# Kernel optimization log

Hardware: AMD Instinct MI355X
Metric: run time of the kernel (lower is better)

The kernel has to match this reference:

```python
import jax, jax.numpy as jnp
import numpy as np

B, H, W, C = 32, 56, 56, 192
WS, SH = 7, 3            # window size, shift size
NH = 6                   # num heads
HD = C // NH             # head dim = 32
N = WS * WS              # tokens per window = 49
NW = (H // WS) * (W // WS)  # windows per image = 64
HID = int(C * 4.0)       # MLP hidden = 768
EPS = 1e-6               # flax LayerNorm default


def _rel_index():
    # (N, N) int index into the (2*WS-1)^2 relative position bias table
    coords = np.stack(np.meshgrid(np.arange(WS), np.arange(WS), indexing='ij')).reshape(2, -1)
    rel = coords[:, :, None] - coords[:, None, :]          # (2, N, N)
    rel = rel.transpose(1, 2, 0) + (WS - 1)                # shift to >= 0
    idx = rel[..., 0] * (2 * WS - 1) + rel[..., 1]
    return jnp.asarray(idx, jnp.int32)


def _attn_mask():
    # standard Swin shifted-window mask: -100 between different regions
    img = np.zeros((H, W))
    cnt = 0
    for hs in (slice(0, -WS), slice(-WS, -SH), slice(-SH, None)):
        for ws in (slice(0, -WS), slice(-WS, -SH), slice(-SH, None)):
            img[hs, ws] = cnt
            cnt += 1
    win = img.reshape(H // WS, WS, W // WS, WS).transpose(0, 2, 1, 3).reshape(NW, N)
    diff = win[:, None, :] - win[:, :, None]
    return jnp.asarray(np.where(diff != 0, -100.0, 0.0), jnp.float32)


def setup_inputs() -> dict:
    key = jax.random.key(0)
    ks = jax.random.split(key, 8)
    s = 0.02
    return {
        'x': jax.random.normal(ks[0], (B, H, W, C), jnp.float32),
        'mask': _attn_mask(),
        'rel_index': _rel_index(),
        'ln1_scale': jnp.ones((C,), jnp.float32),
        'ln1_bias': jnp.zeros((C,), jnp.float32),
        'qkv_w': jax.random.normal(ks[1], (C, 3 * C), jnp.float32) * s,
        'qkv_b': jnp.zeros((3 * C,), jnp.float32),
        'rpb_table': jax.random.normal(ks[2], ((2 * WS - 1) ** 2, NH), jnp.float32) * s,
        'proj_w': jax.random.normal(ks[3], (C, C), jnp.float32) * s,
        'proj_b': jnp.zeros((C,), jnp.float32),
        'ln2_scale': jnp.ones((C,), jnp.float32),
        'ln2_bias': jnp.zeros((C,), jnp.float32),
        'mlp_w1': jax.random.normal(ks[4], (C, HID), jnp.float32) * s,
        'mlp_b1': jnp.zeros((HID,), jnp.float32),
        'mlp_w2': jax.random.normal(ks[5], (HID, C), jnp.float32) * s,
        'mlp_b2': jnp.zeros((C,), jnp.float32),
    }


def _ln(x, scale, bias):
    mu = jnp.mean(x, axis=-1, keepdims=True)
    var = jnp.mean(jnp.square(x - mu), axis=-1, keepdims=True)
    return (x - mu) * jax.lax.rsqrt(var + EPS) * scale + bias


def reference(x, mask, rel_index, ln1_scale, ln1_bias, qkv_w, qkv_b, rpb_table,
              proj_w, proj_b, ln2_scale, ln2_bias, mlp_w1, mlp_b1, mlp_w2, mlp_b2):
    # ---- W-MSA branch ----
    y = _ln(x, ln1_scale, ln1_bias)
    # cyclic shift (grid divisible by window -> pad_to_blocks is a no-op)
    y = jnp.roll(y, shift=(-SH, -SH), axis=(1, 2))
    # window partition: (B,H,W,C) -> (B*NW, N, C)
    y = y.reshape(B, H // WS, WS, W // WS, WS, C).transpose(0, 1, 3, 2, 4, 5)
    y = y.reshape(B * NW, N, C)
    # qkv: (B*NW, N, 3, NH, HD) -> q,k,v each (B*NW, NH, N, HD)
    qkv = (y @ qkv_w + qkv_b).reshape(B * NW, N, 3, NH, HD).transpose(2, 0, 3, 1, 4)
    q, k, v = qkv[0], qkv[1], qkv[2]
    attn = jnp.einsum('bhnd,bhmd->bhnm', q, k) * (HD ** -0.5)
    # relative position bias: (N,N,NH) -> (1,NH,N,N)
    attn = attn + rpb_table[rel_index].transpose(2, 0, 1)[None]
    # shifted-window mask: broadcast over batch and heads
    attn = attn.reshape(B, NW, NH, N, N) + mask[None, :, None]
    attn = jax.nn.softmax(attn.reshape(B * NW, NH, N, N), axis=-1)
    y = jnp.einsum('bhnm,bhmd->bhnd', attn, v).transpose(0, 2, 1, 3).reshape(B * NW, N, C)
    y = y @ proj_w + proj_b
    # window reverse and un-shift
    y = y.reshape(B, H // WS, W // WS, WS, WS, C).transpose(0, 1, 3, 2, 4, 5).reshape(B, H, W, C)
    y = jnp.roll(y, shift=(SH, SH), axis=(1, 2))
    x = x + y
    # ---- MLP branch ----
    z = _ln(x, ln2_scale, ln2_bias)
    z = jax.nn.gelu(z @ mlp_w1 + mlp_b1)  # flax nn.gelu default (tanh approx)
    z = z @ mlp_w2 + mlp_b2
    return x + z
```

## Files before the change

kernel.cpp:

```cpp
#include <hip/hip_runtime.h>


typedef __bf16 bf16_t;
typedef __bf16 bf16x8 __attribute__((ext_vector_type(8)));
typedef float  f32x4  __attribute__((ext_vector_type(4)));

__device__ inline float wred_sum(float v) {
#pragma unroll
  for (int o = 32; o; o >>= 1) v += __shfl_xor(v, o);
  return v;
}

__device__ inline float gelu_tanh(float x) {
  float u = 0.7978845608028654f * (x + 0.044715f * x * x * x);
  float e = __expf(2.f * u);
  float t = 1.f - 2.f / (e + 1.f);
  return 0.5f * x * (1.f + t);
}

__global__ __launch_bounds__(256) void k_ln1_win(
    const float* __restrict__ x, const float* __restrict__ sc,
    const float* __restrict__ bi, bf16_t* __restrict__ yw, int b0, int nTok) {
  int wv = (int)((blockIdx.x * 256 + threadIdx.x) >> 6);
  int lane = threadIdx.x & 63;
  if (wv >= nTok) return;
  int winL = wv / 49;
  int t = wv - winL * 49;
  int wi = winL & 63;
  int b = b0 + (winL >> 6);
  int t7 = t / 7;
  int hr = (wi >> 3) * 7 + t7;
  int wr = (wi & 7) * 7 + (t - t7 * 7);
  int h = hr + 3; if (h >= 56) h -= 56;
  int w = wr + 3; if (w >= 56) w -= 56;
  const float* xp = x + (((size_t)(b * 56 + h)) * 56 + w) * 192;
  float v0 = xp[lane], v1 = xp[lane + 64], v2 = xp[lane + 128];
  float s = wred_sum(v0 + v1 + v2);
  float q = wred_sum(v0 * v0 + v1 * v1 + v2 * v2);
  float mu = s * (1.f / 192.f);
  float var = q * (1.f / 192.f) - mu * mu;
  float rs = rsqrtf(var + 1e-6f);
  bf16_t* op = yw + (size_t)wv * 192;
  op[lane]       = (bf16_t)((v0 - mu) * rs * sc[lane]       + bi[lane]);
  op[lane + 64]  = (bf16_t)((v1 - mu) * rs * sc[lane + 64]  + bi[lane + 64]);
  op[lane + 128] = (bf16_t)((v2 - mu) * rs * sc[lane + 128] + bi[lane + 128]);
}

__global__ __launch_bounds__(256) void k_transpose_cvt(
    const float* __restrict__ in, bf16_t* __restrict__ out, int K, int N) {
  int idx = blockIdx.x * 256 + threadIdx.x;
  if (idx >= K * N) return;
  int n = idx / K, k = idx - n * K;
  out[idx] = (bf16_t)in[(size_t)k * N + n];
}

template <int K>
__global__ __launch_bounds__(256, 2) void k_gemm_bs(
    const bf16_t* __restrict__ A, const bf16_t* __restrict__ Bt,
    const float* __restrict__ bias, bf16_t* __restrict__ C, int Nn, int nMt) {
  constexpr int NKS = K / 32;
  int tid = threadIdx.x;
  int w = tid >> 6, lane = tid & 63;
  int c = lane & 15, g = lane >> 4;
  int bn = blockIdx.x;
  bf16x8 bf[4][NKS];
  const bf16_t* bp = Bt + (size_t)(bn * 64 + c) * K + 8 * g;
#pragma unroll
  for (int jc = 0; jc < 4; ++jc)
#pragma unroll
    for (int ks = 0; ks < NKS; ++ks)
      bf[jc][ks] = *(const bf16x8*)(bp + (size_t)jc * 16 * K + 32 * ks);
  float4 bias4[4];
#pragma unroll
  for (int jc = 0; jc < 4; ++jc)
    bias4[jc] = *(const float4*)(bias + bn * 64 + jc * 16 + 4 * g);
  for (int mt = blockIdx.y; mt < nMt; mt += gridDim.y) {
    int m0 = mt * 256 + w * 64;
    f32x4 acc[4][4] = {};
    const bf16_t* ap = A + (size_t)(m0 + c) * K + 8 * g;
#pragma unroll
    for (int ks = 0; ks < NKS; ++ks) {
      bf16x8 af[4];
#pragma unroll
      for (int ir = 0; ir < 4; ++ir)
        af[ir] = *(const bf16x8*)(ap + (size_t)ir * 16 * K + 32 * ks);
#pragma unroll
      for (int jc = 0; jc < 4; ++jc)
#pragma unroll
        for (int ir = 0; ir < 4; ++ir)
          acc[jc][ir] = __builtin_amdgcn_mfma_f32_16x16x32_bf16(
              bf[jc][ks], af[ir], acc[jc][ir], 0, 0, 0);
    }
#pragma unroll
    for (int ir = 0; ir < 4; ++ir) {
      bf16_t* cp = C + (size_t)(m0 + ir * 16 + c) * Nn + bn * 64 + 4 * g;
#pragma unroll
      for (int jc = 0; jc < 4; ++jc) {
        union { uint2 u; bf16_t e[4]; } pk;
#pragma unroll
        for (int r = 0; r < 4; ++r)
          pk.e[r] = (bf16_t)(acc[jc][ir][r] + ((const float*)&bias4[jc])[r]);
        *(uint2*)(cp + jc * 16) = pk.u;
      }
    }
  }
}

__global__ __launch_bounds__(64) void k_attn(
    const bf16_t* __restrict__ qkv, const int* __restrict__ relidx,
    const float* __restrict__ rpb, const float* __restrict__ mask,
    bf16_t* __restrict__ attn_out) {
  __shared__ char sm[8192];
  int blk = blockIdx.x;
  int wL = blk / 6, h = blk - wL * 6;
  int lane = threadIdx.x;
  int c = lane & 15, g = lane >> 4;
  {
    const float* mw = mask + (size_t)(wL & 63) * 2401;
    __bf16* bl = (__bf16*)sm;
    for (int idx = lane; idx < 2401; idx += 64)
      bl[idx] = (__bf16)(rpb[relidx[idx] * 6 + h] + mw[idx]);
  }
  const bf16_t* baseq = qkv + (size_t)wL * (49 * 576);
  f32x4 s[4][4] = {};
  bf16x8 qf[4], kf[4];
#pragma unroll
  for (int i = 0; i < 4; ++i) {
    int n = c + 16 * i; if (n > 48) n = 48;
    qf[i] = *(const bf16x8*)(baseq + (size_t)n * 576 + h * 32 + g * 8);
  }
#pragma unroll
  for (int j = 0; j < 4; ++j) {
    int m = c + 16 * j; if (m > 48) m = 48;
    kf[j] = *(const bf16x8*)(baseq + (size_t)m * 576 + 192 + h * 32 + g * 8);
  }
#pragma unroll
  for (int i = 0; i < 4; ++i)
#pragma unroll
    for (int j = 0; j < 4; ++j)
      s[i][j] = __builtin_amdgcn_mfma_f32_16x16x32_bf16(qf[i], kf[j], s[i][j],
                                                        0, 0, 0);
  const __bf16* bl = (const __bf16*)sm;
  float mxv[4][4], sum[4][4];
#pragma unroll
  for (int i = 0; i < 4; ++i)
#pragma unroll
    for (int r = 0; r < 4; ++r) {
      int n = 16 * i + 4 * g + r;
      int nc = n > 48 ? 48 : n;
      float best = -1e30f;
#pragma unroll
      for (int j = 0; j < 4; ++j) {
        int m = 16 * j + c;
        float v = -1e30f;
        if (m < 49)
          v = s[i][j][r] * 0.17677669529663687f + (float)bl[nc * 49 + m];
        s[i][j][r] = v;
        best = fmaxf(best, v);
      }
      mxv[i][r] = best;
    }
#pragma unroll
  for (int o = 8; o; o >>= 1)
#pragma unroll
    for (int i = 0; i < 4; ++i)
#pragma unroll
      for (int r = 0; r < 4; ++r)
        mxv[i][r] = fmaxf(mxv[i][r], __shfl_xor(mxv[i][r], o));
#pragma unroll
  for (int i = 0; i < 4; ++i)
#pragma unroll
    for (int r = 0; r < 4; ++r) {
      float ss = 0.f;
#pragma unroll
      for (int j = 0; j < 4; ++j) {
        float p = __expf(s[i][j][r] - mxv[i][r]);
        s[i][j][r] = p;
        ss += p;
      }
      sum[i][r] = ss;
    }
#pragma unroll
  for (int o = 8; o; o >>= 1)
#pragma unroll
    for (int i = 0; i < 4; ++i)
#pragma unroll
      for (int r = 0; r < 4; ++r)
        sum[i][r] += __shfl_xor(sum[i][r], o);
#pragma unroll
  for (int i = 0; i < 4; ++i)
#pragma unroll
    for (int j = 0; j < 4; ++j)
#pragma unroll
      for (int r = 0; r < 4; ++r) {
        int n = 16 * i + 4 * g + r;
        int m = 16 * j + c;
        int offb = n * 128 + ((2 * m) ^ ((n & 7) << 4));
        *(__bf16*)(sm + offb) = (__bf16)s[i][j][r];
      }
  f32x4 o2[4][2] = {};
#pragma unroll
  for (int kt = 0; kt < 2; ++kt) {
    bf16x8 pf[4], vf[2];
#pragma unroll
    for (int i = 0; i < 4; ++i) {
      int n = c + 16 * i;
      int cb = (16 * g + 64 * kt) ^ ((n & 7) << 4);
      pf[i] = *(const bf16x8*)(sm + n * 128 + cb);
    }
#pragma unroll
    for (int dt = 0; dt < 2; ++dt) {
      int d = c + 16 * dt;
      union { bf16x8 v; __bf16 e[8]; } u;
#pragma unroll
      for (int e0 = 0; e0 < 8; ++e0) {
        int m = 8 * g + e0 + 32 * kt; if (m > 48) m = 48;
        u.e[e0] = baseq[(size_t)m * 576 + 384 + h * 32 + d];
      }
      vf[dt] = u.v;
    }
#pragma unroll
    for (int i = 0; i < 4; ++i)
#pragma unroll
      for (int dt = 0; dt < 2; ++dt)
        o2[i][dt] = __builtin_amdgcn_mfma_f32_16x16x32_bf16(pf[i], vf[dt],
                                                            o2[i][dt], 0, 0, 0);
  }
#pragma unroll
  for (int i = 0; i < 4; ++i)
#pragma unroll
    for (int dt = 0; dt < 2; ++dt)
#pragma unroll
      for (int r = 0; r < 4; ++r) {
        int n = 16 * i + 4 * g + r;
        if (n < 49) {
          int d = 16 * dt + c;
          attn_out[((size_t)wL * 49 + n) * 192 + h * 32 + d] =
              (bf16_t)(o2[i][dt][r] / sum[i][r]);
        }
      }
}

__global__ __launch_bounds__(256) void k_unwin_ln2(
    const float* __restrict__ x, const bf16_t* __restrict__ projw,
    const float* __restrict__ sc, const float* __restrict__ bi,
    float* __restrict__ out, bf16_t* __restrict__ z, int b0, int nTok) {
  int wv = (int)((blockIdx.x * 256 + threadIdx.x) >> 6);
  int lane = threadIdx.x & 63;
  if (wv >= nTok) return;
  int bL = wv / 3136;
  int rem = wv - bL * 3136;
  int hh = rem / 56, ww2 = rem - hh * 56;
  int b = b0 + bL;
  int hr = hh + 53; if (hr >= 56) hr -= 56;
  int wr = ww2 + 53; if (wr >= 56) wr -= 56;
  int winL = bL * 64 + (hr / 7) * 8 + (wr / 7);
  int t = (hr % 7) * 7 + (wr % 7);
  const bf16_t* pp = projw + ((size_t)winL * 49 + t) * 192;
  size_t gtok = ((size_t)(b * 56 + hh)) * 56 + ww2;
  const float* xp = x + gtok * 192;
  float v0 = xp[lane]       + (float)pp[lane];
  float v1 = xp[lane + 64]  + (float)pp[lane + 64];
  float v2 = xp[lane + 128] + (float)pp[lane + 128];
  float* op = out + gtok * 192;
  op[lane] = v0; op[lane + 64] = v1; op[lane + 128] = v2;
  float s = wred_sum(v0 + v1 + v2);
  float q = wred_sum(v0 * v0 + v1 * v1 + v2 * v2);
  float mu = s * (1.f / 192.f);
  float var = q * (1.f / 192.f) - mu * mu;
  float rs = rsqrtf(var + 1e-6f);
  bf16_t* zp = z + gtok * 192;
  zp[lane]       = (bf16_t)((v0 - mu) * rs * sc[lane]       + bi[lane]);
  zp[lane + 64]  = (bf16_t)((v1 - mu) * rs * sc[lane + 64]  + bi[lane + 64]);
  zp[lane + 128] = (bf16_t)((v2 - mu) * rs * sc[lane + 128] + bi[lane + 128]);
}

__global__ __launch_bounds__(256, 2) void k_mlp_fused(
    const bf16_t* __restrict__ z, const bf16_t* __restrict__ w1T,
    const float* __restrict__ b1, const bf16_t* __restrict__ w2T,
    const float* __restrict__ b2, float* __restrict__ out) {
  __shared__ char hsm[128 * 256];
  int tid = threadIdx.x;
  int w = tid >> 6, lane = tid & 63;
  int c = lane & 15, g = lane >> 4;
  int wr = w >> 1, wc = w & 1;
  int m0 = blockIdx.x * 128;
  f32x4 acc2[6][4] = {};
  for (int hc = 0; hc < 6; ++hc) {
    f32x4 acc1[4][4] = {};
    const bf16_t* zp = z + (size_t)(m0 + wr * 64 + c) * 192 + 8 * g;
    const bf16_t* w1p = w1T + (size_t)(hc * 128 + wc * 64 + c) * 192 + 8 * g;
#pragma unroll
    for (int ks = 0; ks < 6; ++ks) {
      bf16x8 zf[4], wf[4];
#pragma unroll
      for (int i = 0; i < 4; ++i) {
        zf[i] = *(const bf16x8*)(zp + (size_t)i * 16 * 192 + 32 * ks);
        wf[i] = *(const bf16x8*)(w1p + (size_t)i * 16 * 192 + 32 * ks);
      }
#pragma unroll
      for (int jh = 0; jh < 4; ++jh)
#pragma unroll
        for (int ir = 0; ir < 4; ++ir)
          acc1[jh][ir] = __builtin_amdgcn_mfma_f32_16x16x32_bf16(
              wf[jh], zf[ir], acc1[jh][ir], 0, 0, 0);
    }
    if (hc) __syncthreads();
#pragma unroll
    for (int jh = 0; jh < 4; ++jh) {
      float4 b1v = *(const float4*)(b1 + hc * 128 + wc * 64 + jh * 16 + 4 * g);
#pragma unroll
      for (int ir = 0; ir < 4; ++ir) {
        union { uint2 u; __bf16 e[4]; } pk;
#pragma unroll
        for (int r = 0; r < 4; ++r)
          pk.e[r] = (__bf16)gelu_tanh(acc1[jh][ir][r] + ((const float*)&b1v)[r]);
        int row = wr * 64 + ir * 16 + c;
        int byo = (wc * 64 + jh * 16 + 4 * g) * 2;
        *(uint2*)(hsm + row * 256 + (byo ^ ((row & 7) << 4))) = pk.u;
      }
    }
    __syncthreads();
    const bf16_t* w2p = w2T + (size_t)(wc * 96 + c) * 768 + hc * 128 + 8 * g;
#pragma unroll
    for (int ks = 0; ks < 4; ++ks) {
      bf16x8 hf[4], wf2[6];
#pragma unroll
      for (int ir = 0; ir < 4; ++ir) {
        int row = wr * 64 + ir * 16 + c;
        int byo = 16 * g + 64 * ks;
        hf[ir] = *(const bf16x8*)(hsm + row * 256 + (byo ^ ((row & 7) << 4)));
      }
#pragma unroll
      for (int jc = 0; jc < 6; ++jc)
        wf2[jc] = *(const bf16x8*)(w2p + (size_t)jc * 16 * 768 + 32 * ks);
#pragma unroll
      for (int jc = 0; jc < 6; ++jc)
#pragma unroll
        for (int ir = 0; ir < 4; ++ir)
          acc2[jc][ir] = __builtin_amdgcn_mfma_f32_16x16x32_bf16(
              wf2[jc], hf[ir], acc2[jc][ir], 0, 0, 0);
    }
  }
#pragma unroll
  for (int jc = 0; jc < 6; ++jc) {
    float4 b2v = *(const float4*)(b2 + wc * 96 + jc * 16 + 4 * g);
#pragma unroll
    for (int ir = 0; ir < 4; ++ir) {
      int row = m0 + wr * 64 + ir * 16 + c;
      float* op = out + (size_t)row * 192 + wc * 96 + jc * 16 + 4 * g;
      float4 cur = *(float4*)op;
      cur.x += acc2[jc][ir][0] + b2v.x;
      cur.y += acc2[jc][ir][1] + b2v.y;
      cur.z += acc2[jc][ir][2] + b2v.z;
      cur.w += acc2[jc][ir][3] + b2v.w;
      *(float4*)op = cur;
    }
  }
}

extern "C" void kernel_launch(void* const* d_in, const int* in_sizes, int n_in,
                              void* d_out, int out_size, void* d_ws,
                              size_t ws_size, hipStream_t stream) {
  (void)in_sizes; (void)n_in; (void)out_size;
  const float* x     = (const float*)d_in[0];
  const float* maskp = (const float*)d_in[1];
  const int*   reli  = (const int*)d_in[2];
  const float* ln1s  = (const float*)d_in[3];
  const float* ln1b  = (const float*)d_in[4];
  const float* qkvw  = (const float*)d_in[5];
  const float* qkvb  = (const float*)d_in[6];
  const float* rpb   = (const float*)d_in[7];
  const float* projw = (const float*)d_in[8];
  const float* projb = (const float*)d_in[9];
  const float* ln2s  = (const float*)d_in[10];
  const float* ln2b  = (const float*)d_in[11];
  const float* w1    = (const float*)d_in[12];
  const float* b1    = (const float*)d_in[13];
  const float* w2    = (const float*)d_in[14];
  const float* b2    = (const float*)d_in[15];
  float* out = (float*)d_out;

  auto aup = [](size_t v) { return (v + 255) & ~(size_t)255; };
  char* base = (char*)d_ws;
  size_t off = 0;
  bf16_t* z_buf = (bf16_t*)(base + off); off += aup((size_t)100352 * 192 * 2);
  bf16_t* qkvT  = (bf16_t*)(base + off); off += aup((size_t)576 * 192 * 2);
  bf16_t* projT = (bf16_t*)(base + off); off += aup((size_t)192 * 192 * 2);
  bf16_t* w1T   = (bf16_t*)(base + off); off += aup((size_t)768 * 192 * 2);
  bf16_t* w2T   = (bf16_t*)(base + off); off += aup((size_t)192 * 768 * 2);
  size_t offB = off;

  int Bc = 32;
  while (Bc > 4 && offB + (size_t)Bc * 3136 * (576 + 192) * 2 > ws_size)
    Bc >>= 1;
  bf16_t* bufB = (bf16_t*)(base + offB);
  bf16_t* bufA = (bf16_t*)(base + offB + aup((size_t)Bc * 3136 * 576 * 2));

  k_transpose_cvt<<<(192 * 576 + 255) / 256, 256, 0, stream>>>(qkvw, qkvT, 192, 576);
  k_transpose_cvt<<<(192 * 192 + 255) / 256, 256, 0, stream>>>(projw, projT, 192, 192);
  k_transpose_cvt<<<(192 * 768 + 255) / 256, 256, 0, stream>>>(w1, w1T, 192, 768);
  k_transpose_cvt<<<(768 * 192 + 255) / 256, 256, 0, stream>>>(w2, w2T, 768, 192);

  for (int b0 = 0; b0 < 32; b0 += Bc) {
    int nTok = Bc * 3136, nWin = Bc * 64;
    int nMt = nTok / 256;
    k_ln1_win<<<nTok / 4, 256, 0, stream>>>(x, ln1s, ln1b, bufA, b0, nTok);
    {
      int nbn = 576 / 64;
      int gy = (512 + nbn - 1) / nbn; if (gy > nMt) gy = nMt;
      k_gemm_bs<192><<<dim3(nbn, gy), 256, 0, stream>>>(bufA, qkvT, qkvb, bufB,
                                                        576, nMt);
    }
    k_attn<<<nWin * 6, 64, 0, stream>>>(bufB, reli, rpb, maskp, bufA);
    {
      int nbn = 192 / 64;
      int gy = (512 + nbn - 1) / nbn; if (gy > nMt) gy = nMt;
      k_gemm_bs<192><<<dim3(nbn, gy), 256, 0, stream>>>(bufA, projT, projb,
                                                        bufB, 192, nMt);
    }
    k_unwin_ln2<<<nTok / 4, 256, 0, stream>>>(x, bufB, ln2s, ln2b, out, z_buf,
                                              b0, nTok);
  }

  k_mlp_fused<<<100352 / 128, 256, 0, stream>>>(z_buf, w1T, b1, w2T, b2, out);
}
```

Before: 678.6 us.

## Restructure fused MLP so each wave owns 32 rows with private LDS

Rewrites the fused MLP kernel so each wave handles 32 token rows across the full hidden and output width, instead of a 2x2 split of a 128-row tile. The z fragments are loaded into registers once and reused over all hidden chunks. Each wave writes its GELU activations to a private 4 KB LDS slice, which removes the block-wide __syncthreads. In exchange, every wave now reloads its own copy of the w1/w2 weights with less reuse per load, and the 12x2 accumulator array raises register pressure.

```diff
diff --git a/kernel.cpp b/kernel.cpp
--- a/kernel.cpp
+++ b/kernel.cpp
@@ -275,80 +275,86 @@
   zp[lane + 128] = (bf16_t)((v2 - mu) * rs * sc[lane + 128] + bi[lane + 128]);
 }
 
-__global__ __launch_bounds__(256, 2) void k_mlp_fused(
+__global__ __launch_bounds__(256, 2) void k_mlp_fused2(
     const bf16_t* __restrict__ z, const bf16_t* __restrict__ w1T,
     const float* __restrict__ b1, const bf16_t* __restrict__ w2T,
     const float* __restrict__ b2, float* __restrict__ out) {
-  __shared__ char hsm[128 * 256];
+  __shared__ char hsm[16384];
   int tid = threadIdx.x;
-  int w = tid >> 6, lane = tid & 63;
+  int wv = tid >> 6, lane = tid & 63;
   int c = lane & 15, g = lane >> 4;
-  int wr = w >> 1, wc = w & 1;
-  int m0 = blockIdx.x * 128;
-  f32x4 acc2[6][4] = {};
-  for (int hc = 0; hc < 6; ++hc) {
-    f32x4 acc1[4][4] = {};
-    const bf16_t* zp = z + (size_t)(m0 + wr * 64 + c) * 192 + 8 * g;
-    const bf16_t* w1p = w1T + (size_t)(hc * 128 + wc * 64 + c) * 192 + 8 * g;
+  char* wbase = hsm + wv * 4096;
+  int row0 = blockIdx.x * 128 + wv * 32;
+
+  bf16x8 zfr[2][6];
+  const bf16_t* zp = z + (size_t)(row0 + c) * 192 + 8 * g;
+#pragma unroll
+  for (int ir = 0; ir < 2; ++ir)
+#pragma unroll
+    for (int ks = 0; ks < 6; ++ks)
+      zfr[ir][ks] = *(const bf16x8*)(zp + (size_t)ir * 16 * 192 + 32 * ks);
+
+  f32x4 acc2[12][2] = {};
+
+  for (int hc = 0; hc < 12; ++hc) {
+    f32x4 acc1[4][2] = {};
+    const bf16_t* w1p = w1T + (size_t)(hc * 64 + c) * 192 + 8 * g;
 #pragma unroll
     for (int ks = 0; ks < 6; ++ks) {
-      bf16x8 zf[4], wf[4];
-#pragma unroll
-      for (int i = 0; i < 4; ++i) {
-        zf[i] = *(const bf16x8*)(zp + (size_t)i * 16 * 192 + 32 * ks);
-        wf[i] = *(const bf16x8*)(w1p + (size_t)i * 16 * 192 + 32 * ks);
-      }
+      bf16x8 wf[4];
 #pragma unroll
       for (int jh = 0; jh < 4; ++jh)
-#pragma unroll
-        for (int ir = 0; ir < 4; ++ir)
+        wf[jh] = *(const bf16x8*)(w1p + (size_t)jh * 16 * 192 + 32 * ks);
+#pragma unroll
+      for (int jh = 0; jh < 4; ++jh)
+#pragma unroll
+        for (int ir = 0; ir < 2; ++ir)
           acc1[jh][ir] = __builtin_amdgcn_mfma_f32_16x16x32_bf16(
-              wf[jh], zf[ir], acc1[jh][ir], 0, 0, 0);
-    }
-    if (hc) __syncthreads();
+              wf[jh], zfr[ir][ks], acc1[jh][ir], 0, 0, 0);
+    }
 #pragma unroll
     for (int jh = 0; jh < 4; ++jh) {
-      float4 b1v = *(const float4*)(b1 + hc * 128 + wc * 64 + jh * 16 + 4 * g);
-#pragma unroll
-      for (int ir = 0; ir < 4; ++ir) {
+      float4 b1v = *(const float4*)(b1 + hc * 64 + jh * 16 + 4 * g);
+#pragma unroll
+      for (int ir = 0; ir < 2; ++ir) {
         union { uint2 u; __bf16 e[4]; } pk;
 #pragma unroll
         for (int r = 0; r < 4; ++r)
           pk.e[r] = (__bf16)gelu_tanh(acc1[jh][ir][r] + ((const float*)&b1v)[r]);
-        int row = wr * 64 + ir * 16 + c;
-        int byo = (wc * 64 + jh * 16 + 4 * g) * 2;
-        *(uint2*)(hsm + row * 256 + (byo ^ ((row & 7) << 4))) = pk.u;
-      }
-    }
-    __syncthreads();
-    const bf16_t* w2p = w2T + (size_t)(wc * 96 + c) * 768 + hc * 128 + 8 * g;
-#pragma unroll
-    for (int ks = 0; ks < 4; ++ks) {
-      bf16x8 hf[4], wf2[6];
-#pragma unroll
-      for (int ir = 0; ir < 4; ++ir) {
-        int row = wr * 64 + ir * 16 + c;
-        int byo = 16 * g + 64 * ks;
-        hf[ir] = *(const bf16x8*)(hsm + row * 256 + (byo ^ ((row & 7) << 4)));
-      }
-#pragma unroll
-      for (int jc = 0; jc < 6; ++jc)
-        wf2[jc] = *(const bf16x8*)(w2p + (size_t)jc * 16 * 768 + 32 * ks);
-#pragma unroll
-      for (int jc = 0; jc < 6; ++jc)
-#pragma unroll
-        for (int ir = 0; ir < 4; ++ir)
+        int rl = ir * 16 + c;
+        *(uint2*)(wbase + rl * 128 + ((32 * jh + 8 * g) ^ ((rl & 7) << 4))) =
+            pk.u;
+      }
+    }
+    const bf16_t* w2p = w2T + (size_t)c * 768 + hc * 64 + 8 * g;
+#pragma unroll
+    for (int ks2 = 0; ks2 < 2; ++ks2) {
+      bf16x8 af[2];
+#pragma unroll
+      for (int ir = 0; ir < 2; ++ir) {
+        int rl = ir * 16 + c;
+        af[ir] = *(const bf16x8*)(wbase + rl * 128 +
+                                  ((64 * ks2 + 16 * g) ^ ((rl & 7) << 4)));
+      }
+      bf16x8 wf2[12];
+#pragma unroll
+      for (int jc = 0; jc < 12; ++jc)
+        wf2[jc] = *(const bf16x8*)(w2p + (size_t)jc * 16 * 768 + 32 * ks2);
+#pragma unroll
+      for (int jc = 0; jc < 12; ++jc)
+#pragma unroll
+        for (int ir = 0; ir < 2; ++ir)
           acc2[jc][ir] = __builtin_amdgcn_mfma_f32_16x16x32_bf16(
-              wf2[jc], hf[ir], acc2[jc][ir], 0, 0, 0);
-    }
-  }
-#pragma unroll
-  for (int jc = 0; jc < 6; ++jc) {
-    float4 b2v = *(const float4*)(b2 + wc * 96 + jc * 16 + 4 * g);
-#pragma unroll
-    for (int ir = 0; ir < 4; ++ir) {
-      int row = m0 + wr * 64 + ir * 16 + c;
-      float* op = out + (size_t)row * 192 + wc * 96 + jc * 16 + 4 * g;
+              wf2[jc], af[ir], acc2[jc][ir], 0, 0, 0);
+    }
+  }
+#pragma unroll
+  for (int jc = 0; jc < 12; ++jc) {
+    float4 b2v = *(const float4*)(b2 + jc * 16 + 4 * g);
+#pragma unroll
+    for (int ir = 0; ir < 2; ++ir) {
+      int row = row0 + ir * 16 + c;
+      float* op = out + (size_t)row * 192 + jc * 16 + 4 * g;
       float4 cur = *(float4*)op;
       cur.x += acc2[jc][ir][0] + b2v.x;
       cur.y += acc2[jc][ir][1] + b2v.y;
@@ -423,5 +429,5 @@
                                               b0, nTok);
   }
 
-  k_mlp_fused<<<100352 / 128, 256, 0, stream>>>(z_buf, w1T, b1, w2T, b2, out);
-}
+  k_mlp_fused2<<<100352 / 128, 256, 0, stream>>>(z_buf, w1T, b1, w2T, b2, out);
+}
```

New measurement: 755.5 us. +11.3%, slower.
